# Kernel optimization log

Measured on AMD Instinct MI355X. Metric: run time of the kernel, lower is better.

The kernel has to match this reference:

```python
import jax, jax.numpy as jnp
import numpy as np
import math

B, T, C, H = 4, 2048, 768, 12
HS = C // H  # 64


def setup_inputs() -> dict:
    key = jax.random.key(0)
    ks = jax.random.split(key, 6)
    s = 1.0 / math.sqrt(C)
    return {
        "x": jax.random.normal(ks[0], (B, T, C), dtype=jnp.float32),
        "memory": jax.random.normal(ks[1], (B, T, C), dtype=jnp.float32),
        "Wq": jax.random.normal(ks[2], (C, C), dtype=jnp.float32) * s,
        "bq": jnp.zeros((C,), dtype=jnp.float32),
        "Wkv": jax.random.normal(ks[3], (C, 2 * C), dtype=jnp.float32) * s,
        "bkv": jnp.zeros((2 * C,), dtype=jnp.float32),
        "Wproj": jax.random.normal(ks[4], (C, C), dtype=jnp.float32) * s,
        "bproj": jnp.zeros((C,), dtype=jnp.float32),
    }


def reference(x, memory, Wq, bq, Wkv, bkv, Wproj, bproj):
    # q projection of decoder stream x, kv projection of encoder memory
    q = x @ Wq + bq                      # [B,T,C]
    kv = memory @ Wkv + bkv              # [B,T,2C]
    k, v = jnp.split(kv, 2, axis=2)      # [B,T,C] each

    def heads(t):
        return t.reshape(B, T, H, HS).transpose(0, 2, 1, 3)  # [B,H,T,hs]

    q, k, v = heads(q), heads(k), heads(v)
    scale = 1.0 / math.sqrt(HS)
    att = jnp.einsum("bhqd,bhkd->bhqk", q, k) * scale        # [B,H,T,T]
    att = jax.nn.softmax(att, axis=-1)
    y = jnp.einsum("bhqk,bhkd->bhqd", att, v)                # [B,H,T,hs]
    y = y.transpose(0, 2, 1, 3).reshape(B, T, C)
    return y @ Wproj + bproj
```

## Files before the change

kernel.cpp:

```cpp
#include <hip/hip_runtime.h>
#include <hip/hip_bf16.h>


#define B_  4
#define T_  2048
#define C_  768
#define H_  12
#define HS_ 64

typedef __attribute__((ext_vector_type(8))) short short8;
typedef __attribute__((ext_vector_type(4))) float f32x4;

__device__ __forceinline__ short f2bf(float f) {
    __hip_bfloat16 h = __float2bfloat16(f);
    return *reinterpret_cast<short*>(&h);
}

__device__ __forceinline__ void gload_lds16(const void* g, void* l) {
    __builtin_amdgcn_global_load_lds((const __attribute__((address_space(1))) void*)g,
                                     (__attribute__((address_space(3))) void*)l,
                                     16, 0, 0);
}


__global__ void prepass(const float* __restrict__ x, short* __restrict__ xb,
                        const float* __restrict__ mem, short* __restrict__ memb,
                        const float* __restrict__ Wq,  short* __restrict__ WqT,
                        const float* __restrict__ Wkv, short* __restrict__ WkvT,
                        const float* __restrict__ Wp,  short* __restrict__ WpT,
                        float qscale) {
    const int n4 = 8192 * 768 / 4;
    const int cvtblocks = (2 * n4) / 256;
    int bid = blockIdx.x;
    if (bid < cvtblocks) {
        int i = bid * 256 + threadIdx.x;
        const float* in; short* out;
        if (i < n4) { in = x; out = xb; }
        else        { in = mem; out = memb; i -= n4; }
        float4 v = reinterpret_cast<const float4*>(in)[i];
        short4 o;
        o.x = f2bf(v.x); o.y = f2bf(v.y); o.z = f2bf(v.z); o.w = f2bf(v.w);
        reinterpret_cast<short4*>(out)[i] = o;
        return;
    }
    __shared__ float tile[32][33];
    bid -= cvtblocks;
    const float* in; short* out; int N; float sc = 1.0f;
    if (bid < 576)       { in = Wq;  out = WqT;  N = 768;  sc = qscale; }
    else if (bid < 1728) { in = Wkv; out = WkvT; N = 1536; bid -= 576; }
    else                 { in = Wp;  out = WpT;  N = 768;  bid -= 1728; }
    const int tiles_n = N >> 5;
    const int k0 = (bid / tiles_n) * 32;
    const int n0 = (bid % tiles_n) * 32;
    const int r = threadIdx.x >> 5;
    const int c = threadIdx.x & 31;
    #pragma unroll
    for (int i = 0; i < 4; ++i)
        tile[r + 8 * i][c] = in[(size_t)(k0 + r + 8 * i) * N + n0 + c];
    __syncthreads();
    #pragma unroll
    for (int i = 0; i < 4; ++i)
        out[(size_t)(n0 + r + 8 * i) * 768 + k0 + c] = f2bf(tile[c][r + 8 * i] * sc);
}


template<int OUT_F32, int WRITE_VT>
__device__ __forceinline__ void gemm_body(const short* __restrict__ A, const short* __restrict__ BT,
                                          const float* __restrict__ bias, void* __restrict__ out,
                                          short* __restrict__ vt,
                                          int m0, int n0, int K, int ldo, float bscale,
                                          short (*As)[64], short (*Bs)[64]) {
    const int t  = threadIdx.x;
    const int wid = t >> 6;
    const int wm = wid >> 1, wn = wid & 1;
    const int lane = t & 63;
    const int lr = lane & 15;
    const int lk = (lane >> 4) * 8;

    f32x4 acc[4][4] = {};

    const int srow = wid * 32 + (lane >> 3);
    const int scol = (lane & 7) * 8;

    for (int k0 = 0; k0 < K; k0 += 64) {
        __syncthreads();
        #pragma unroll
        for (int i = 0; i < 4; ++i)
            gload_lds16(&A[(size_t)(m0 + srow + i * 8) * K + k0 + scol],
                        &As[wid * 32 + i * 8][0]);
        #pragma unroll
        for (int i = 0; i < 4; ++i)
            gload_lds16(&BT[(size_t)(n0 + srow + i * 8) * K + k0 + scol],
                        &Bs[wid * 32 + i * 8][0]);
        __syncthreads();

        #pragma unroll
        for (int ks = 0; ks < 2; ++ks) {
            const int kk = ks * 32 + lk;
            short8 a[4], b[4];
            #pragma unroll
            for (int m = 0; m < 4; ++m)
                a[m] = *reinterpret_cast<const short8*>(&As[wm*64 + m*16 + lr][kk]);
            #pragma unroll
            for (int n = 0; n < 4; ++n)
                b[n] = *reinterpret_cast<const short8*>(&Bs[wn*64 + n*16 + lr][kk]);
            #pragma unroll
            for (int m = 0; m < 4; ++m)
                #pragma unroll
                for (int n = 0; n < 4; ++n)
                    acc[m][n] = __builtin_amdgcn_mfma_f32_16x16x32_bf16(a[m], b[n], acc[m][n], 0, 0, 0);
        }
    }

    const int rb = m0 + wm * 64;
    const int cb = n0 + wn * 64;
    const int rj = (lane >> 4) * 4;
    #pragma unroll
    for (int n = 0; n < 4; ++n) {
        const int col = cb + n * 16 + lr;
        const float bv = bias[col] * bscale;
        #pragma unroll
        for (int m = 0; m < 4; ++m) {
            #pragma unroll
            for (int j = 0; j < 4; ++j) {
                const int row = rb + m * 16 + rj + j;
                const float v = acc[m][n][j] + bv;
                if (WRITE_VT && col >= 768) {
                    const int vd = col - 768;
                    const int hh = vd >> 6, dd = vd & 63;
                    const int bb = row >> 11, tt = row & 2047;
                    const int kv = tt & 63;
                    const int slot = 32 * (kv >> 5) + 8 * ((kv >> 2) & 3)
                                   + 4 * ((kv >> 4) & 1) + (kv & 3);
                    const int ptt = (tt & ~63) | slot;
                    vt[(((size_t)bb * H_ + hh) * HS_ + dd) * T_ + ptt] = f2bf(v);
                } else if (OUT_F32) {
                    reinterpret_cast<float*>(out)[(size_t)row * ldo + col] = v;
                } else {
                    reinterpret_cast<short*>(out)[(size_t)row * ldo + col] = f2bf(v);
                }
            }
        }
    }
}

__global__ void gemm_qkv(const short* __restrict__ xb,  const short* __restrict__ memb,
                         const short* __restrict__ WqT, const short* __restrict__ WkvT,
                         const float* __restrict__ bq,  const float* __restrict__ bkv,
                         short* __restrict__ qb, short* __restrict__ kvb,
                         short* __restrict__ vt, float qscale) {
    __shared__ short As[128][64];
    __shared__ short Bs[128][64];
    const int lin = blockIdx.y * 18 + blockIdx.x;
    const int swz = (lin % 8) * 144 + lin / 8;
    const int bx = swz % 18;
    const int m0 = (swz / 18) * 128;
    if (bx < 6) {
        gemm_body<0,0>(xb, WqT, bq, qb, nullptr, m0, bx * 128, 768, 768, qscale, As, Bs);
    } else {
        gemm_body<0,1>(memb, WkvT, bkv, kvb, vt, m0, (bx - 6) * 128, 768, 1536, 1.0f, As, Bs);
    }
}

__global__ void gemm_out(const short* __restrict__ yb, const short* __restrict__ WpT,
                         const float* __restrict__ bproj, float* __restrict__ out) {
    __shared__ short As[128][64];
    __shared__ short Bs[128][64];
    const int lin = blockIdx.y * 6 + blockIdx.x;
    const int swz = (lin % 8) * 48 + lin / 8;
    gemm_body<1,0>(yb, WpT, bproj, out, nullptr, (swz / 6) * 128, (swz % 6) * 128,
                   768, 768, 1.0f, As, Bs);
}


__global__ void __launch_bounds__(256)
attn_fwd12(const short* __restrict__ qb, const short* __restrict__ kvb,
           const short* __restrict__ vtb, short* __restrict__ yb) {
    __shared__ short Ks[64][72];
    __shared__ short Vt[64][72];

    const int id = blockIdx.x;
    const int pair = id % 48;
    const int b = pair / H_, h = pair % H_;
    const int q0 = (id / 48) * 128;
    const int t = threadIdx.x;
    const int w = t >> 6;
    const int lane = t & 63;
    const int lr = lane & 15;
    const int g = lane >> 4;

    const int str = t >> 2;
    const int stc = (t & 3) * 16;

    const short* Kb = kvb + (size_t)b * T_ * (2 * C_) + h * HS_;
    const short* Vb = vtb + (size_t)(b * H_ + h) * HS_ * T_;

    short8 aq[2][2];
    #pragma unroll
    for (int m = 0; m < 2; ++m)
        #pragma unroll
        for (int ks = 0; ks < 2; ++ks)
            aq[m][ks] = *reinterpret_cast<const short8*>(
                &qb[(size_t)(b * T_ + q0 + w * 32 + m * 16 + lr) * C_ + h * HS_ + ks * 32 + g * 8]);

    short8 ones8;
    #pragma unroll
    for (int i = 0; i < 8; ++i) ones8[i] = (short)0x3F80;

    f32x4 acc[2][4] = {};
    f32x4 accl[2] = {};

    uint4 kr0, kr1, vr0, vr1;
    {
        const short* gk = &Kb[(size_t)str * (2 * C_) + stc];
        const short* gv = &Vb[(size_t)str * T_ + stc];
        kr0 = *reinterpret_cast<const uint4*>(gk);
        kr1 = *reinterpret_cast<const uint4*>(gk + 8);
        vr0 = *reinterpret_cast<const uint4*>(gv);
        vr1 = *reinterpret_cast<const uint4*>(gv + 8);
    }

    for (int kv0 = 0; kv0 < T_; kv0 += 64) {
        __syncthreads();
        *reinterpret_cast<uint4*>(&Ks[str][stc])     = kr0;
        *reinterpret_cast<uint4*>(&Ks[str][stc + 8]) = kr1;
        *reinterpret_cast<uint4*>(&Vt[str][stc])     = vr0;
        *reinterpret_cast<uint4*>(&Vt[str][stc + 8]) = vr1;
        __syncthreads();

        if (kv0 + 64 < T_) {
            const short* gk = &Kb[(size_t)(kv0 + 64 + str) * (2 * C_) + stc];
            const short* gv = &Vb[(size_t)str * T_ + kv0 + 64 + stc];
            kr0 = *reinterpret_cast<const uint4*>(gk);
            kr1 = *reinterpret_cast<const uint4*>(gk + 8);
            vr0 = *reinterpret_cast<const uint4*>(gv);
            vr1 = *reinterpret_cast<const uint4*>(gv + 8);
        }

        f32x4 s[2][4] = {};
        #pragma unroll
        for (int ks = 0; ks < 2; ++ks) {
            #pragma unroll
            for (int n = 0; n < 4; ++n) {
                short8 bk = *reinterpret_cast<const short8*>(&Ks[n * 16 + lr][ks * 32 + g * 8]);
                #pragma unroll
                for (int m = 0; m < 2; ++m)
                    s[m][n] = __builtin_amdgcn_mfma_f32_16x16x32_bf16(bk, aq[m][ks], s[m][n], 0, 0, 0);
            }
        }

        short8 pa[2][2];
        #pragma unroll
        for (int m = 0; m < 2; ++m) {
            #pragma unroll
            for (int n = 0; n < 4; ++n) {
                #pragma unroll
                for (int j = 0; j < 4; ++j)
                    s[m][n][j] = exp2f(s[m][n][j]);
            }
            #pragma unroll
            for (int ks = 0; ks < 2; ++ks) {
                pa[m][ks][0] = f2bf(s[m][2*ks][0]); pa[m][ks][1] = f2bf(s[m][2*ks][1]);
                pa[m][ks][2] = f2bf(s[m][2*ks][2]); pa[m][ks][3] = f2bf(s[m][2*ks][3]);
                pa[m][ks][4] = f2bf(s[m][2*ks+1][0]); pa[m][ks][5] = f2bf(s[m][2*ks+1][1]);
                pa[m][ks][6] = f2bf(s[m][2*ks+1][2]); pa[m][ks][7] = f2bf(s[m][2*ks+1][3]);
            }
        }

        #pragma unroll
        for (int ks = 0; ks < 2; ++ks) {
            #pragma unroll
            for (int m = 0; m < 2; ++m)
                accl[m] = __builtin_amdgcn_mfma_f32_16x16x32_bf16(pa[m][ks], ones8, accl[m], 0, 0, 0);
            #pragma unroll
            for (int n = 0; n < 4; ++n) {
                short8 bv = *reinterpret_cast<const short8*>(&Vt[n * 16 + lr][ks * 32 + g * 8]);
                #pragma unroll
                for (int m = 0; m < 2; ++m)
                    acc[m][n] = __builtin_amdgcn_mfma_f32_16x16x32_bf16(pa[m][ks], bv, acc[m][n], 0, 0, 0);
            }
        }
    }

    #pragma unroll
    for (int m = 0; m < 2; ++m) {
        #pragma unroll
        for (int j = 0; j < 4; ++j) {
            const float inv = 1.f / accl[m][j];
            const size_t row = (size_t)(b * T_ + q0 + w * 32 + m * 16 + g * 4 + j);
            #pragma unroll
            for (int n = 0; n < 4; ++n)
                yb[row * C_ + h * HS_ + n * 16 + lr] = f2bf(acc[m][n][j] * inv);
        }
    }
}


extern "C" void kernel_launch(void* const* d_in, const int* in_sizes, int n_in,
                              void* d_out, int out_size, void* d_ws, size_t ws_size,
                              hipStream_t stream) {
    const float* x      = (const float*)d_in[0];
    const float* memory = (const float*)d_in[1];
    const float* Wq     = (const float*)d_in[2];
    const float* bq     = (const float*)d_in[3];
    const float* Wkv    = (const float*)d_in[4];
    const float* bkv    = (const float*)d_in[5];
    const float* Wproj  = (const float*)d_in[6];
    const float* bproj  = (const float*)d_in[7];

    char* ws = (char*)d_ws;
    size_t off = 0;
    auto alloc = [&](size_t bytes) { char* p = ws + off; off += (bytes + 255) & ~(size_t)255; return p; };
    short* xb   = (short*)alloc((size_t)8192 * 768 * 2);
    short* memb = (short*)alloc((size_t)8192 * 768 * 2);
    short* qb   = (short*)alloc((size_t)8192 * 768 * 2);
    short* kvb  = (short*)alloc((size_t)8192 * 1536 * 2);
    short* vtb  = (short*)alloc((size_t)B_ * H_ * HS_ * T_ * 2);
    short* WqT  = (short*)alloc((size_t)768 * 768 * 2);
    short* WkvT = (short*)alloc((size_t)1536 * 768 * 2);
    short* WpT  = (short*)alloc((size_t)768 * 768 * 2);

    const float qscale = 1.4426950408889634f / 8.0f;

    prepass<<<12288 + 2304, 256, 0, stream>>>(x, xb, memory, memb,
                                              Wq, WqT, Wkv, WkvT, Wproj, WpT, qscale);
    gemm_qkv<<<dim3(18, 64), 256, 0, stream>>>(xb, memb, WqT, WkvT, bq, bkv, qb, kvb, vtb, qscale);
    attn_fwd12<<<dim3(16 * 48), 256, 0, stream>>>(qb, kvb, vtb, xb );
    gemm_out<<<dim3(6, 64), 256, 0, stream>>>(xb, WpT, bproj, (float*)d_out);
}
```

Measured before the change: 174.3 us.

## Double-buffer attention K/V via direct global-to-LDS loads with XOR-swizzled layouts

The QKV GEMM now writes K into a per-head contiguous [B,H,T,64] buffer and V into the transposed buffer, both with an XOR swizzle baked in. The attention kernel replaces its register-staged K/V prefetch and padded LDS tiles with global_load_lds into double-buffered, unpadded shared tiles, reading them through the matching swizzle. This is meant to remove the register round trip and one barrier per chunk, avoid LDS bank conflicts without padding, and overlap the next tile's load with compute. The cost is more scattered stores in the GEMM epilogue and an extra LDS buffer.

New measurement: 168.5 us. 3.4% less time.

```diff
diff --git a/kernel.cpp b/kernel.cpp
--- a/kernel.cpp
+++ b/kernel.cpp
@@ -64,10 +64,10 @@
 }
 
 
-template<int OUT_F32, int WRITE_VT>
+template<int OUT_F32, int WRITE_KV>
 __device__ __forceinline__ void gemm_body(const short* __restrict__ A, const short* __restrict__ BT,
                                           const float* __restrict__ bias, void* __restrict__ out,
-                                          short* __restrict__ vt,
+                                          short* __restrict__ kt, short* __restrict__ vt,
                                           int m0, int n0, int K, int ldo, float bscale,
                                           short (*As)[64], short (*Bs)[64]) {
     const int t  = threadIdx.x;
@@ -125,15 +125,21 @@
             for (int j = 0; j < 4; ++j) {
                 const int row = rb + m * 16 + rj + j;
                 const float v = acc[m][n][j] + bv;
-                if (WRITE_VT && col >= 768) {
-                    const int vd = col - 768;
-                    const int hh = vd >> 6, dd = vd & 63;
+                if (WRITE_KV) {
                     const int bb = row >> 11, tt = row & 2047;
-                    const int kv = tt & 63;
-                    const int slot = 32 * (kv >> 5) + 8 * ((kv >> 2) & 3)
-                                   + 4 * ((kv >> 4) & 1) + (kv & 3);
-                    const int ptt = (tt & ~63) | slot;
-                    vt[(((size_t)bb * H_ + hh) * HS_ + dd) * T_ + ptt] = f2bf(v);
+                    if (col < 768) {
+                        const int hh = col >> 6, dd = col & 63;
+                        const int s = ((((dd >> 3) ^ (tt & 7)) << 3) | (dd & 7));
+                        kt[(((size_t)bb * H_ + hh) * T_ + tt) * 64 + s] = f2bf(v);
+                    } else {
+                        const int vd = col - 768;
+                        const int hh = vd >> 6, dd = vd & 63;
+                        const int kv = tt & 63;
+                        const int slot = 32 * (kv >> 5) + 8 * ((kv >> 2) & 3)
+                                       + 4 * ((kv >> 4) & 1) + (kv & 3);
+                        const int slot2 = (((slot >> 3) ^ (dd & 7)) << 3) | (slot & 7);
+                        vt[(((size_t)bb * H_ + hh) * HS_ + dd) * T_ + (tt & ~63) + slot2] = f2bf(v);
+                    }
                 } else if (OUT_F32) {
                     reinterpret_cast<float*>(out)[(size_t)row * ldo + col] = v;
                 } else {
@@ -147,7 +153,7 @@
 __global__ void gemm_qkv(const short* __restrict__ xb,  const short* __restrict__ memb,
                          const short* __restrict__ WqT, const short* __restrict__ WkvT,
                          const float* __restrict__ bq,  const float* __restrict__ bkv,
-                         short* __restrict__ qb, short* __restrict__ kvb,
+                         short* __restrict__ qb, short* __restrict__ kt,
                          short* __restrict__ vt, float qscale) {
     __shared__ short As[128][64];
     __shared__ short Bs[128][64];
@@ -156,9 +162,9 @@
     const int bx = swz % 18;
     const int m0 = (swz / 18) * 128;
     if (bx < 6) {
-        gemm_body<0,0>(xb, WqT, bq, qb, nullptr, m0, bx * 128, 768, 768, qscale, As, Bs);
+        gemm_body<0,0>(xb, WqT, bq, qb, nullptr, nullptr, m0, bx * 128, 768, 768, qscale, As, Bs);
     } else {
-        gemm_body<0,1>(memb, WkvT, bkv, kvb, vt, m0, (bx - 6) * 128, 768, 1536, 1.0f, As, Bs);
+        gemm_body<0,1>(memb, WkvT, bkv, nullptr, kt, vt, m0, (bx - 6) * 128, 768, 1536, 1.0f, As, Bs);
     }
 }
 
@@ -168,16 +174,16 @@
     __shared__ short Bs[128][64];
     const int lin = blockIdx.y * 6 + blockIdx.x;
     const int swz = (lin % 8) * 48 + lin / 8;
-    gemm_body<1,0>(yb, WpT, bproj, out, nullptr, (swz / 6) * 128, (swz % 6) * 128,
+    gemm_body<1,0>(yb, WpT, bproj, out, nullptr, nullptr, (swz / 6) * 128, (swz % 6) * 128,
                    768, 768, 1.0f, As, Bs);
 }
 
 
 __global__ void __launch_bounds__(256)
-attn_fwd12(const short* __restrict__ qb, const short* __restrict__ kvb,
+attn_fwd15(const short* __restrict__ qb, const short* __restrict__ ktb,
            const short* __restrict__ vtb, short* __restrict__ yb) {
-    __shared__ short Ks[64][72];
-    __shared__ short Vt[64][72];
+    __shared__ short Ks[2][64][64];
+    __shared__ short Vt[2][64][64];
 
     const int id = blockIdx.x;
     const int pair = id % 48;
@@ -189,10 +195,7 @@
     const int lr = lane & 15;
     const int g = lane >> 4;
 
-    const int str = t >> 2;
-    const int stc = (t & 3) * 16;
-
-    const short* Kb = kvb + (size_t)b * T_ * (2 * C_) + h * HS_;
+    const short* Kb = ktb + (size_t)(b * H_ + h) * T_ * 64;
     const short* Vb = vtb + (size_t)(b * H_ + h) * HS_ * T_;
 
     short8 aq[2][2];
@@ -210,39 +213,27 @@
     f32x4 acc[2][4] = {};
     f32x4 accl[2] = {};
 
-    uint4 kr0, kr1, vr0, vr1;
-    {
-        const short* gk = &Kb[(size_t)str * (2 * C_) + stc];
-        const short* gv = &Vb[(size_t)str * T_ + stc];
-        kr0 = *reinterpret_cast<const uint4*>(gk);
-        kr1 = *reinterpret_cast<const uint4*>(gk + 8);
-        vr0 = *reinterpret_cast<const uint4*>(gv);
-        vr1 = *reinterpret_cast<const uint4*>(gv + 8);
-    }
-
-    for (int kv0 = 0; kv0 < T_; kv0 += 64) {
+    auto stage = [&](int kv0, int c) {
+        #pragma unroll
+        for (int i = 0; i < 2; ++i) {
+            gload_lds16(Kb + (size_t)(kv0 + w * 16 + i * 8 + (lane >> 3)) * 64 + (lane & 7) * 8,
+                        &Ks[c][w * 16 + i * 8][0]);
+            gload_lds16(Vb + (size_t)(w * 16 + i * 8 + (lane >> 3)) * T_ + kv0 + (lane & 7) * 8,
+                        &Vt[c][w * 16 + i * 8][0]);
+        }
+    };
+
+    auto chunk = [&](int kv0, int c) {
         __syncthreads();
-        *reinterpret_cast<uint4*>(&Ks[str][stc])     = kr0;
-        *reinterpret_cast<uint4*>(&Ks[str][stc + 8]) = kr1;
-        *reinterpret_cast<uint4*>(&Vt[str][stc])     = vr0;
-        *reinterpret_cast<uint4*>(&Vt[str][stc + 8]) = vr1;
-        __syncthreads();
-
-        if (kv0 + 64 < T_) {
-            const short* gk = &Kb[(size_t)(kv0 + 64 + str) * (2 * C_) + stc];
-            const short* gv = &Vb[(size_t)str * T_ + kv0 + 64 + stc];
-            kr0 = *reinterpret_cast<const uint4*>(gk);
-            kr1 = *reinterpret_cast<const uint4*>(gk + 8);
-            vr0 = *reinterpret_cast<const uint4*>(gv);
-            vr1 = *reinterpret_cast<const uint4*>(gv + 8);
-        }
+        if (kv0 + 64 < T_) stage(kv0 + 64, c ^ 1);
 
         f32x4 s[2][4] = {};
         #pragma unroll
         for (int ks = 0; ks < 2; ++ks) {
             #pragma unroll
             for (int n = 0; n < 4; ++n) {
-                short8 bk = *reinterpret_cast<const short8*>(&Ks[n * 16 + lr][ks * 32 + g * 8]);
+                short8 bk = *reinterpret_cast<const short8*>(
+                    &Ks[c][n * 16 + lr][(((ks * 4 + g) ^ (lr & 7)) << 3)]);
                 #pragma unroll
                 for (int m = 0; m < 2; ++m)
                     s[m][n] = __builtin_amdgcn_mfma_f32_16x16x32_bf16(bk, aq[m][ks], s[m][n], 0, 0, 0);
@@ -274,12 +265,19 @@
                 accl[m] = __builtin_amdgcn_mfma_f32_16x16x32_bf16(pa[m][ks], ones8, accl[m], 0, 0, 0);
             #pragma unroll
             for (int n = 0; n < 4; ++n) {
-                short8 bv = *reinterpret_cast<const short8*>(&Vt[n * 16 + lr][ks * 32 + g * 8]);
+                short8 bv = *reinterpret_cast<const short8*>(
+                    &Vt[c][n * 16 + lr][(((ks * 4 + g) ^ (lr & 7)) << 3)]);
                 #pragma unroll
                 for (int m = 0; m < 2; ++m)
                     acc[m][n] = __builtin_amdgcn_mfma_f32_16x16x32_bf16(pa[m][ks], bv, acc[m][n], 0, 0, 0);
             }
         }
+    };
+
+    stage(0, 0);
+    for (int kv0 = 0; kv0 < T_; kv0 += 128) {
+        chunk(kv0, 0);
+        chunk(kv0 + 64, 1);
     }
 
     #pragma unroll
@@ -314,7 +312,7 @@
     short* xb   = (short*)alloc((size_t)8192 * 768 * 2);
     short* memb = (short*)alloc((size_t)8192 * 768 * 2);
     short* qb   = (short*)alloc((size_t)8192 * 768 * 2);
-    short* kvb  = (short*)alloc((size_t)8192 * 1536 * 2);
+    short* ktb  = (short*)alloc((size_t)B_ * H_ * T_ * 64 * 2);
     short* vtb  = (short*)alloc((size_t)B_ * H_ * HS_ * T_ * 2);
     short* WqT  = (short*)alloc((size_t)768 * 768 * 2);
     short* WkvT = (short*)alloc((size_t)1536 * 768 * 2);
@@ -324,7 +322,7 @@
 
     prepass<<<12288 + 2304, 256, 0, stream>>>(x, xb, memory, memb,
                                               Wq, WqT, Wkv, WkvT, Wproj, WpT, qscale);
-    gemm_qkv<<<dim3(18, 64), 256, 0, stream>>>(xb, memb, WqT, WkvT, bq, bkv, qb, kvb, vtb, qscale);
-    attn_fwd12<<<dim3(16 * 48), 256, 0, stream>>>(qb, kvb, vtb, xb );
+    gemm_qkv<<<dim3(18, 64), 256, 0, stream>>>(xb, memb, WqT, WkvT, bq, bkv, qb, ktb, vtb, qscale);
+    attn_fwd15<<<dim3(16 * 48), 256, 0, stream>>>(qb, ktb, vtb, xb );
     gemm_out<<<dim3(6, 64), 256, 0, stream>>>(xb, WpT, bproj, (float*)d_out);
 }
```
